# Performance work log

Measured on AMD Instinct MI355X. Metric: run time of the kernel, lower is better.

## Reference

```python
import jax, jax.numpy as jnp
import numpy as np

A, D, H, NACT = 8, 128, 64, 16  # n_agents, input_shape, rnn_hidden_dim, n_actions
B = 16384


def setup_inputs() -> dict:
    key = jax.random.key(0)
    ks = jax.random.split(key, 12)
    s = 1.0 / np.sqrt(H)
    si = 1.0 / np.sqrt(D)
    inp = {
        'inputs': jax.random.normal(ks[0], (B * A, D), dtype=jnp.float32),
        'hidden_state': jax.random.normal(ks[1], (B, A, H), dtype=jnp.float32),
        # stacked per-agent (non-shared) weights, PyTorch default-init scale
        'W1': jax.random.uniform(ks[2], (A, H, D), jnp.float32, -si, si),
        'b1': jax.random.uniform(ks[3], (A, H), jnp.float32, -si, si),
        'W_ih': jax.random.uniform(ks[4], (A, 3 * H, H), jnp.float32, -s, s),
        'b_ih': jax.random.uniform(ks[5], (A, 3 * H), jnp.float32, -s, s),
        'W_hh': jax.random.uniform(ks[6], (A, 3 * H, H), jnp.float32, -s, s),
        'b_hh': jax.random.uniform(ks[7], (A, 3 * H), jnp.float32, -s, s),
        'W2': jax.random.uniform(ks[8], (A, NACT, H), jnp.float32, -s, s),
        'b2': jax.random.uniform(ks[9], (A, NACT), jnp.float32, -s, s),
    }
    return inp


def reference(inputs, hidden_state, W1, b1, W_ih, b_ih, W_hh, b_hh, W2, b2):
    x = inputs.reshape(-1, A, D)                 # [B, A, D]
    h = hidden_state.reshape(-1, A, H)           # [B, A, H]
    # fc1 + ReLU, batched over agents
    z1 = jax.nn.relu(jnp.einsum('bad,ahd->bah', x, W1) + b1)
    # GRUCell (PyTorch convention: gates r, z, n)
    gi = jnp.einsum('bah,agh->bag', z1, W_ih) + b_ih   # [B, A, 3H]
    gh = jnp.einsum('bah,agh->bag', h, W_hh) + b_hh
    i_r, i_z, i_n = jnp.split(gi, 3, axis=-1)
    h_r, h_z, h_n = jnp.split(gh, 3, axis=-1)
    r = jax.nn.sigmoid(i_r + h_r)
    z = jax.nn.sigmoid(i_z + h_z)
    n = jnp.tanh(i_n + r * h_n)
    h_new = (1.0 - z) * n + z * h                # [B, A, H]
    # fc2
    q = jnp.einsum('bah,anh->ban', h_new, W2) + b2   # [B, A, NACT]
    # match torch: cat(qs, dim=-1).view(-1, n_actions) == reshape [B*A, NACT]
    return q.reshape(-1, NACT), h_new
```

## Files before the change

### kernel.cpp

```cpp
#include <hip/hip_runtime.h>
#include <hip/hip_bf16.h>
#include <cstddef>

#define NAGENT 8
#define DIN    128
#define HID    64
#define NACT   16

typedef __attribute__((ext_vector_type(8))) short bf16x8;
typedef __attribute__((ext_vector_type(4))) float f32x4;

__device__ __forceinline__ short f2bf(float f) {
    __hip_bfloat16 h = __float2bfloat16(f);
    union { __hip_bfloat16 h; short s; } u; u.h = h;
    return u.s;
}
__device__ __forceinline__ float sigmoid_f(float v) { return 1.0f / (1.0f + __expf(-v)); }
__device__ __forceinline__ float tanh_f(float v) {
    v = fminf(fmaxf(v, -15.0f), 15.0f);
    float e = __expf(2.0f * v);
    return (e - 1.0f) / (e + 1.0f);
}
__device__ __forceinline__ bf16x8 cvt8pair(float4 v0, float4 v1) {
    bf16x8 r;
    r[0] = f2bf(v0.x); r[1] = f2bf(v0.y); r[2] = f2bf(v0.z); r[3] = f2bf(v0.w);
    r[4] = f2bf(v1.x); r[5] = f2bf(v1.y); r[6] = f2bf(v1.z); r[7] = f2bf(v1.w);
    return r;
}

extern "C" __global__ void __launch_bounds__(256)
conv_weights_packed(const float* __restrict__ W1, const float* __restrict__ Wih,
                    const float* __restrict__ Whh, const float* __restrict__ W2,
                    short* __restrict__ ws)
{
    const int a = blockIdx.y;
    const int c = blockIdx.x * 256 + threadIdx.x;
    if (c >= 4224) return;
    const int lane = c & 63, lr = lane & 15, lk = lane >> 4;
    const float* src;
    if (c < 1024) {
        int n = c >> 8, k = (c >> 6) & 3;
        src = W1 + a * 8192 + (n * 16 + lr) * 128 + k * 32 + lk * 8;
    } else if (c < 2560) {
        int idx = (c - 1024) >> 6;
        int g = idx >> 3, n = (idx >> 1) & 3, kk = idx & 1;
        src = Wih + a * 12288 + (g * 64 + n * 16 + lr) * 64 + kk * 32 + lk * 8;
    } else if (c < 4096) {
        int idx = (c - 2560) >> 6;
        int g = idx >> 3, n = (idx >> 1) & 3, kk = idx & 1;
        src = Whh + a * 12288 + (g * 64 + n * 16 + lr) * 64 + kk * 32 + lk * 8;
    } else {
        int kk = (c - 4096) >> 6;
        src = W2 + a * 1024 + lr * 64 + kk * 32 + lk * 8;
    }
    float4 v0 = ((const float4*)src)[0];
    float4 v1 = ((const float4*)src)[1];
    bf16x8 o = cvt8pair(v0, v1);
    *(bf16x8*)(ws + (size_t)a * 33792 + (size_t)c * 8) = o;
}

extern "C" __global__ void __launch_bounds__(256, 4)
rnn_main(const float* __restrict__ x,
         const float* __restrict__ hin,
         const float* __restrict__ b1, const float* __restrict__ bih,
         const float* __restrict__ bhh, const float* __restrict__ b2,
         const short* __restrict__ wsp,
         float* __restrict__ qout,
         float* __restrict__ hout)
{
    const int bid  = blockIdx.x;
    const int a    = bid & 7;
    const int t    = threadIdx.x;
    const int wid  = t >> 6;
    const int lane = t & 63;
    const int lr   = lane & 15;
    const int lk   = lane >> 4;

    __shared__ short zs[4 * 1024];
    char* zb = (char*)(zs + wid * 1024);

    const short* wsA = wsp + (size_t)a * 33792;
    const int tile = (bid >> 3) * 4 + wid;
    const int arow = tile * 16 + lr;

    const float* xrow = x + ((size_t)arow * NAGENT + a) * DIN + lk * 8;
    const float* hrow = hin + ((size_t)arow * NAGENT + a) * HID + lk * 8;
    bf16x8 hf0 = cvt8pair(*(const float4*)(hrow),      *(const float4*)(hrow + 4));
    bf16x8 hf1 = cvt8pair(*(const float4*)(hrow + 32), *(const float4*)(hrow + 36));

    {
        f32x4 acc1[4];
        #pragma unroll
        for (int n = 0; n < 4; ++n) {
            float bv = b1[a * HID + n * 16 + lr];
            acc1[n] = (f32x4){bv, bv, bv, bv};
        }
        #pragma unroll
        for (int k = 0; k < 4; ++k) {
            bf16x8 xk = cvt8pair(*(const float4*)(xrow + k * 32),
                                 *(const float4*)(xrow + k * 32 + 4));
            #pragma unroll
            for (int n = 0; n < 4; ++n) {
                bf16x8 wb = *(const bf16x8*)(wsA + ((n * 4 + k) * 64 + lane) * 8);
                acc1[n] = __builtin_amdgcn_mfma_f32_16x16x32_bf16(xk, wb, acc1[n], 0, 0, 0);
            }
        }
        #pragma unroll
        for (int n = 0; n < 4; ++n)
            #pragma unroll
            for (int j = 0; j < 4; ++j) {
                int row = lk * 4 + j, col = n * 16 + lr;
                *(short*)(zb + row * 128 + ((col * 2) ^ ((row & 7) << 4))) =
                    f2bf(fmaxf(acc1[n][j], 0.0f));
            }
    }

    bf16x8 za0 = *(const bf16x8*)(zb + lr * 128 + ((0 * 64 + lk * 16) ^ ((lr & 7) << 4)));
    bf16x8 za1 = *(const bf16x8*)(zb + lr * 128 + ((1 * 64 + lk * 16) ^ ((lr & 7) << 4)));

    #pragma unroll 1
    for (int n = 0; n < 4; ++n) {
        float bhr = bhh[a * 192 +   0 + n * 16 + lr];
        float bhz = bhh[a * 192 +  64 + n * 16 + lr];
        float bhn = bhh[a * 192 + 128 + n * 16 + lr];
        f32x4 aHr = (f32x4){bhr, bhr, bhr, bhr};
        f32x4 aHz = (f32x4){bhz, bhz, bhz, bhz};
        f32x4 aHn = (f32x4){bhn, bhn, bhn, bhn};
        #pragma unroll
        for (int kk = 0; kk < 2; ++kk) {
            bf16x8 hfk = kk ? hf1 : hf0;
            bf16x8 whr = *(const bf16x8*)(wsA + 20480 + (((0 * 4 + n) * 2 + kk) * 64 + lane) * 8);
            bf16x8 whz = *(const bf16x8*)(wsA + 20480 + (((1 * 4 + n) * 2 + kk) * 64 + lane) * 8);
            bf16x8 whn = *(const bf16x8*)(wsA + 20480 + (((2 * 4 + n) * 2 + kk) * 64 + lane) * 8);
            aHr = __builtin_amdgcn_mfma_f32_16x16x32_bf16(hfk, whr, aHr, 0, 0, 0);
            aHz = __builtin_amdgcn_mfma_f32_16x16x32_bf16(hfk, whz, aHz, 0, 0, 0);
            aHn = __builtin_amdgcn_mfma_f32_16x16x32_bf16(hfk, whn, aHn, 0, 0, 0);
        }

        float bir = bih[a * 192 +   0 + n * 16 + lr];
        float biz = bih[a * 192 +  64 + n * 16 + lr];
        float bin_ = bih[a * 192 + 128 + n * 16 + lr];
        f32x4 aIr = (f32x4){bir, bir, bir, bir};
        f32x4 aIz = (f32x4){biz, biz, biz, biz};
        f32x4 aIn = (f32x4){bin_, bin_, bin_, bin_};
        #pragma unroll
        for (int kk = 0; kk < 2; ++kk) {
            bf16x8 zak = kk ? za1 : za0;
            bf16x8 wir = *(const bf16x8*)(wsA + 8192 + (((0 * 4 + n) * 2 + kk) * 64 + lane) * 8);
            bf16x8 wiz = *(const bf16x8*)(wsA + 8192 + (((1 * 4 + n) * 2 + kk) * 64 + lane) * 8);
            bf16x8 win = *(const bf16x8*)(wsA + 8192 + (((2 * 4 + n) * 2 + kk) * 64 + lane) * 8);
            aIr = __builtin_amdgcn_mfma_f32_16x16x32_bf16(zak, wir, aIr, 0, 0, 0);
            aIz = __builtin_amdgcn_mfma_f32_16x16x32_bf16(zak, wiz, aIz, 0, 0, 0);
            aIn = __builtin_amdgcn_mfma_f32_16x16x32_bf16(zak, win, aIn, 0, 0, 0);
        }

        #pragma unroll
        for (int j = 0; j < 4; ++j) {
            int row = lk * 4 + j, col = n * 16 + lr;
            float hp = hin[((size_t)(tile * 16 + row) * NAGENT + a) * HID + col];
            float r  = sigmoid_f(aIr[j] + aHr[j]);
            float zv = sigmoid_f(aIz[j] + aHz[j]);
            float nn = tanh_f(aIn[j] + r * aHn[j]);
            float hv = (1.0f - zv) * nn + zv * hp;
            hout[((size_t)(tile * 16 + row) * NAGENT + a) * HID + col] = hv;
            *(short*)(zb + row * 128 + ((col * 2) ^ ((row & 7) << 4))) = f2bf(hv);
        }
    }

    {
        float bq = b2[a * NACT + lr];
        f32x4 q = (f32x4){bq, bq, bq, bq};
        bf16x8 ha0 = *(const bf16x8*)(zb + lr * 128 + ((0 * 64 + lk * 16) ^ ((lr & 7) << 4)));
        bf16x8 ha1 = *(const bf16x8*)(zb + lr * 128 + ((1 * 64 + lk * 16) ^ ((lr & 7) << 4)));
        bf16x8 w2f0 = *(const bf16x8*)(wsA + 32768 + (0 * 64 + lane) * 8);
        bf16x8 w2f1 = *(const bf16x8*)(wsA + 32768 + (1 * 64 + lane) * 8);
        q = __builtin_amdgcn_mfma_f32_16x16x32_bf16(ha0, w2f0, q, 0, 0, 0);
        q = __builtin_amdgcn_mfma_f32_16x16x32_bf16(ha1, w2f1, q, 0, 0, 0);
        #pragma unroll
        for (int j = 0; j < 4; ++j)
            qout[((size_t)(tile * 16 + lk * 4 + j) * NAGENT + a) * NACT + lr] = q[j];
    }
}

extern "C" void kernel_launch(void* const* d_in, const int* in_sizes, int n_in,
                              void* d_out, int out_size, void* d_ws, size_t ws_size,
                              hipStream_t stream)
{
    const float* x   = (const float*)d_in[0];
    const float* hin = (const float*)d_in[1];
    const float* W1  = (const float*)d_in[2];
    const float* b1  = (const float*)d_in[3];
    const float* Wih = (const float*)d_in[4];
    const float* bih = (const float*)d_in[5];
    const float* Whh = (const float*)d_in[6];
    const float* bhh = (const float*)d_in[7];
    const float* W2  = (const float*)d_in[8];
    const float* b2  = (const float*)d_in[9];

    const int B = in_sizes[0] / (NAGENT * DIN);

    float* qout = (float*)d_out;
    float* hout = (float*)d_out + (size_t)B * NAGENT * NACT;

    short* wsp = (short*)d_ws;

    conv_weights_packed<<<dim3(17, NAGENT), 256, 0, stream>>>(W1, Wih, Whh, W2, wsp);

    dim3 grid((B / 64) * NAGENT);
    rnn_main<<<grid, 256, 0, stream>>>(x, hin, b1, bih, bhh, b2, wsp, qout, hout);
}
```

Before: 48.82 us.

## Switch GRU kernel to 32x32x16 MFMA with 32-row tiles per wave

```diff
diff --git a/kernel.cpp b/kernel.cpp
--- a/kernel.cpp
+++ b/kernel.cpp
@@ -7,8 +7,9 @@
 #define HID    64
 #define NACT   16
 
-typedef __attribute__((ext_vector_type(8))) short bf16x8;
-typedef __attribute__((ext_vector_type(4))) float f32x4;
+typedef __attribute__((ext_vector_type(8)))  short bf16x8;
+typedef __attribute__((ext_vector_type(4)))  float f32x4;
+typedef __attribute__((ext_vector_type(16))) float f32x16;
 
 __device__ __forceinline__ short f2bf(float f) {
     __hip_bfloat16 h = __float2bfloat16(f);
@@ -36,22 +37,24 @@
     const int a = blockIdx.y;
     const int c = blockIdx.x * 256 + threadIdx.x;
     if (c >= 4224) return;
-    const int lane = c & 63, lr = lane & 15, lk = lane >> 4;
+    const int lane  = c & 63;
+    const int chunk = c >> 6;
+    const int l31 = lane & 31, lkk = lane >> 5;
     const float* src;
-    if (c < 1024) {
-        int n = c >> 8, k = (c >> 6) & 3;
-        src = W1 + a * 8192 + (n * 16 + lr) * 128 + k * 32 + lk * 8;
-    } else if (c < 2560) {
-        int idx = (c - 1024) >> 6;
-        int g = idx >> 3, n = (idx >> 1) & 3, kk = idx & 1;
-        src = Wih + a * 12288 + (g * 64 + n * 16 + lr) * 64 + kk * 32 + lk * 8;
-    } else if (c < 4096) {
-        int idx = (c - 2560) >> 6;
-        int g = idx >> 3, n = (idx >> 1) & 3, kk = idx & 1;
-        src = Whh + a * 12288 + (g * 64 + n * 16 + lr) * 64 + kk * 32 + lk * 8;
+    if (chunk < 16) {
+        int n = chunk >> 3, i = chunk & 7;
+        src = W1 + a * 8192 + (n * 32 + l31) * 128 + i * 16 + lkk * 8;
+    } else if (chunk < 40) {
+        int idx = chunk - 16;
+        int g = idx >> 3, cb = (idx >> 2) & 1, ks = idx & 3;
+        src = Wih + a * 12288 + (g * 64 + cb * 32 + l31) * 64 + ks * 16 + lkk * 8;
+    } else if (chunk < 64) {
+        int idx = chunk - 40;
+        int g = idx >> 3, cb = (idx >> 2) & 1, ks = idx & 3;
+        src = Whh + a * 12288 + (g * 64 + cb * 32 + l31) * 64 + ks * 16 + lkk * 8;
     } else {
-        int kk = (c - 4096) >> 6;
-        src = W2 + a * 1024 + lr * 64 + kk * 32 + lk * 8;
+        int kk = chunk - 64;
+        src = W2 + a * 1024 + (lane & 15) * 64 + kk * 32 + (lane >> 4) * 8;
     }
     float4 v0 = ((const float4*)src)[0];
     float4 v1 = ((const float4*)src)[1];
@@ -59,7 +62,7 @@
     *(bf16x8*)(ws + (size_t)a * 33792 + (size_t)c * 8) = o;
 }
 
-extern "C" __global__ void __launch_bounds__(256, 4)
+extern "C" __global__ void __launch_bounds__(256, 2)
 rnn_main(const float* __restrict__ x,
          const float* __restrict__ hin,
          const float* __restrict__ b1, const float* __restrict__ bih,
@@ -73,112 +76,138 @@
     const int t    = threadIdx.x;
     const int wid  = t >> 6;
     const int lane = t & 63;
-    const int lr   = lane & 15;
-    const int lk   = lane >> 4;
-
-    __shared__ short zs[4 * 1024];
-    char* zb = (char*)(zs + wid * 1024);
+    const int l31  = lane & 31;
+    const int lkk  = lane >> 5;
+
+    __shared__ short zs[4 * 2048];
+    char* zb = (char*)(zs + wid * 2048);
 
     const short* wsA = wsp + (size_t)a * 33792;
-    const int tile = (bid >> 3) * 4 + wid;
-    const int arow = tile * 16 + lr;
-
-    const float* xrow = x + ((size_t)arow * NAGENT + a) * DIN + lk * 8;
-    const float* hrow = hin + ((size_t)arow * NAGENT + a) * HID + lk * 8;
-    bf16x8 hf0 = cvt8pair(*(const float4*)(hrow),      *(const float4*)(hrow + 4));
-    bf16x8 hf1 = cvt8pair(*(const float4*)(hrow + 32), *(const float4*)(hrow + 36));
+    const int rbase = ((bid >> 3) * 4 + wid) * 32;
+    const int arow  = rbase + l31;
+
+    const float* xrow = x + ((size_t)arow * NAGENT + a) * DIN + lkk * 8;
+    const float* hrow = hin + ((size_t)arow * NAGENT + a) * HID + lkk * 8;
+
+    bf16x8 hf[4];
+    #pragma unroll
+    for (int ks = 0; ks < 4; ++ks)
+        hf[ks] = cvt8pair(*(const float4*)(hrow + ks * 16),
+                          *(const float4*)(hrow + ks * 16 + 4));
 
     {
-        f32x4 acc1[4];
-        #pragma unroll
-        for (int n = 0; n < 4; ++n) {
-            float bv = b1[a * HID + n * 16 + lr];
-            acc1[n] = (f32x4){bv, bv, bv, bv};
-        }
-        #pragma unroll
-        for (int k = 0; k < 4; ++k) {
-            bf16x8 xk = cvt8pair(*(const float4*)(xrow + k * 32),
-                                 *(const float4*)(xrow + k * 32 + 4));
-            #pragma unroll
-            for (int n = 0; n < 4; ++n) {
-                bf16x8 wb = *(const bf16x8*)(wsA + ((n * 4 + k) * 64 + lane) * 8);
-                acc1[n] = __builtin_amdgcn_mfma_f32_16x16x32_bf16(xk, wb, acc1[n], 0, 0, 0);
-            }
-        }
-        #pragma unroll
-        for (int n = 0; n < 4; ++n)
-            #pragma unroll
-            for (int j = 0; j < 4; ++j) {
-                int row = lk * 4 + j, col = n * 16 + lr;
-                *(short*)(zb + row * 128 + ((col * 2) ^ ((row & 7) << 4))) =
-                    f2bf(fmaxf(acc1[n][j], 0.0f));
-            }
-    }
-
-    bf16x8 za0 = *(const bf16x8*)(zb + lr * 128 + ((0 * 64 + lk * 16) ^ ((lr & 7) << 4)));
-    bf16x8 za1 = *(const bf16x8*)(zb + lr * 128 + ((1 * 64 + lk * 16) ^ ((lr & 7) << 4)));
+        float bv0 = b1[a * HID + l31];
+        float bv1 = b1[a * HID + 32 + l31];
+        f32x16 acc0, acc1;
+        #pragma unroll
+        for (int r = 0; r < 16; ++r) { acc0[r] = bv0; acc1[r] = bv1; }
+        #pragma unroll
+        for (int i = 0; i < 8; ++i) {
+            bf16x8 xa = cvt8pair(*(const float4*)(xrow + i * 16),
+                                 *(const float4*)(xrow + i * 16 + 4));
+            bf16x8 w0 = *(const bf16x8*)(wsA + ((0 * 8 + i) * 64 + lane) * 8);
+            bf16x8 w1 = *(const bf16x8*)(wsA + ((1 * 8 + i) * 64 + lane) * 8);
+            acc0 = __builtin_amdgcn_mfma_f32_32x32x16_bf16(xa, w0, acc0, 0, 0, 0);
+            acc1 = __builtin_amdgcn_mfma_f32_32x32x16_bf16(xa, w1, acc1, 0, 0, 0);
+        }
+        #pragma unroll
+        for (int r = 0; r < 16; ++r) {
+            int row = (r & 3) + 8 * (r >> 2) + 4 * lkk;
+            int c0 = l31, c1 = 32 + l31;
+            *(short*)(zb + row * 128 + ((c0 * 2) ^ ((row & 7) << 4))) =
+                f2bf(fmaxf(acc0[r], 0.0f));
+            *(short*)(zb + row * 128 + ((c1 * 2) ^ ((row & 7) << 4))) =
+                f2bf(fmaxf(acc1[r], 0.0f));
+        }
+    }
+
+    bf16x8 za[4];
+    #pragma unroll
+    for (int ks = 0; ks < 4; ++ks)
+        za[ks] = *(const bf16x8*)(zb + l31 * 128 +
+                                  ((ks * 32 + lkk * 16) ^ ((l31 & 7) << 4)));
 
     #pragma unroll 1
-    for (int n = 0; n < 4; ++n) {
-        float bhr = bhh[a * 192 +   0 + n * 16 + lr];
-        float bhz = bhh[a * 192 +  64 + n * 16 + lr];
-        float bhn = bhh[a * 192 + 128 + n * 16 + lr];
-        f32x4 aHr = (f32x4){bhr, bhr, bhr, bhr};
-        f32x4 aHz = (f32x4){bhz, bhz, bhz, bhz};
-        f32x4 aHn = (f32x4){bhn, bhn, bhn, bhn};
-        #pragma unroll
-        for (int kk = 0; kk < 2; ++kk) {
-            bf16x8 hfk = kk ? hf1 : hf0;
-            bf16x8 whr = *(const bf16x8*)(wsA + 20480 + (((0 * 4 + n) * 2 + kk) * 64 + lane) * 8);
-            bf16x8 whz = *(const bf16x8*)(wsA + 20480 + (((1 * 4 + n) * 2 + kk) * 64 + lane) * 8);
-            bf16x8 whn = *(const bf16x8*)(wsA + 20480 + (((2 * 4 + n) * 2 + kk) * 64 + lane) * 8);
-            aHr = __builtin_amdgcn_mfma_f32_16x16x32_bf16(hfk, whr, aHr, 0, 0, 0);
-            aHz = __builtin_amdgcn_mfma_f32_16x16x32_bf16(hfk, whz, aHz, 0, 0, 0);
-            aHn = __builtin_amdgcn_mfma_f32_16x16x32_bf16(hfk, whn, aHn, 0, 0, 0);
-        }
-
-        float bir = bih[a * 192 +   0 + n * 16 + lr];
-        float biz = bih[a * 192 +  64 + n * 16 + lr];
-        float bin_ = bih[a * 192 + 128 + n * 16 + lr];
-        f32x4 aIr = (f32x4){bir, bir, bir, bir};
-        f32x4 aIz = (f32x4){biz, biz, biz, biz};
-        f32x4 aIn = (f32x4){bin_, bin_, bin_, bin_};
-        #pragma unroll
-        for (int kk = 0; kk < 2; ++kk) {
-            bf16x8 zak = kk ? za1 : za0;
-            bf16x8 wir = *(const bf16x8*)(wsA + 8192 + (((0 * 4 + n) * 2 + kk) * 64 + lane) * 8);
-            bf16x8 wiz = *(const bf16x8*)(wsA + 8192 + (((1 * 4 + n) * 2 + kk) * 64 + lane) * 8);
-            bf16x8 win = *(const bf16x8*)(wsA + 8192 + (((2 * 4 + n) * 2 + kk) * 64 + lane) * 8);
-            aIr = __builtin_amdgcn_mfma_f32_16x16x32_bf16(zak, wir, aIr, 0, 0, 0);
-            aIz = __builtin_amdgcn_mfma_f32_16x16x32_bf16(zak, wiz, aIz, 0, 0, 0);
-            aIn = __builtin_amdgcn_mfma_f32_16x16x32_bf16(zak, win, aIn, 0, 0, 0);
-        }
-
-        #pragma unroll
-        for (int j = 0; j < 4; ++j) {
-            int row = lk * 4 + j, col = n * 16 + lr;
-            float hp = hin[((size_t)(tile * 16 + row) * NAGENT + a) * HID + col];
-            float r  = sigmoid_f(aIr[j] + aHr[j]);
-            float zv = sigmoid_f(aIz[j] + aHz[j]);
-            float nn = tanh_f(aIn[j] + r * aHn[j]);
-            float hv = (1.0f - zv) * nn + zv * hp;
-            hout[((size_t)(tile * 16 + row) * NAGENT + a) * HID + col] = hv;
-            *(short*)(zb + row * 128 + ((col * 2) ^ ((row & 7) << 4))) = f2bf(hv);
+    for (int cb = 0; cb < 2; ++cb) {
+        const int col = cb * 32 + l31;
+        f32x16 rv, zv;
+
+        {
+            float bh = bhh[a * 192 + 0 * 64 + col];
+            float bi = bih[a * 192 + 0 * 64 + col];
+            f32x16 aH, aI;
+            #pragma unroll
+            for (int r = 0; r < 16; ++r) { aH[r] = bh; aI[r] = bi; }
+            #pragma unroll
+            for (int ks = 0; ks < 4; ++ks) {
+                bf16x8 wh = *(const bf16x8*)(wsA + ((40 + (0 * 2 + cb) * 4 + ks) * 64 + lane) * 8);
+                bf16x8 wi = *(const bf16x8*)(wsA + ((16 + (0 * 2 + cb) * 4 + ks) * 64 + lane) * 8);
+                aH = __builtin_amdgcn_mfma_f32_32x32x16_bf16(hf[ks], wh, aH, 0, 0, 0);
+                aI = __builtin_amdgcn_mfma_f32_32x32x16_bf16(za[ks], wi, aI, 0, 0, 0);
+            }
+            #pragma unroll
+            for (int r = 0; r < 16; ++r) rv[r] = sigmoid_f(aI[r] + aH[r]);
+        }
+        {
+            float bh = bhh[a * 192 + 1 * 64 + col];
+            float bi = bih[a * 192 + 1 * 64 + col];
+            f32x16 aH, aI;
+            #pragma unroll
+            for (int r = 0; r < 16; ++r) { aH[r] = bh; aI[r] = bi; }
+            #pragma unroll
+            for (int ks = 0; ks < 4; ++ks) {
+                bf16x8 wh = *(const bf16x8*)(wsA + ((40 + (1 * 2 + cb) * 4 + ks) * 64 + lane) * 8);
+                bf16x8 wi = *(const bf16x8*)(wsA + ((16 + (1 * 2 + cb) * 4 + ks) * 64 + lane) * 8);
+                aH = __builtin_amdgcn_mfma_f32_32x32x16_bf16(hf[ks], wh, aH, 0, 0, 0);
+                aI = __builtin_amdgcn_mfma_f32_32x32x16_bf16(za[ks], wi, aI, 0, 0, 0);
+            }
+            #pragma unroll
+            for (int r = 0; r < 16; ++r) zv[r] = sigmoid_f(aI[r] + aH[r]);
+        }
+        {
+            float bh = bhh[a * 192 + 2 * 64 + col];
+            float bi = bih[a * 192 + 2 * 64 + col];
+            f32x16 aH, aI;
+            #pragma unroll
+            for (int r = 0; r < 16; ++r) { aH[r] = bh; aI[r] = bi; }
+            #pragma unroll
+            for (int ks = 0; ks < 4; ++ks) {
+                bf16x8 wh = *(const bf16x8*)(wsA + ((40 + (2 * 2 + cb) * 4 + ks) * 64 + lane) * 8);
+                bf16x8 wi = *(const bf16x8*)(wsA + ((16 + (2 * 2 + cb) * 4 + ks) * 64 + lane) * 8);
+                aH = __builtin_amdgcn_mfma_f32_32x32x16_bf16(hf[ks], wh, aH, 0, 0, 0);
+                aI = __builtin_amdgcn_mfma_f32_32x32x16_bf16(za[ks], wi, aI, 0, 0, 0);
+            }
+            #pragma unroll
+            for (int r = 0; r < 16; ++r) {
+                int row = (r & 3) + 8 * (r >> 2) + 4 * lkk;
+                float hp = hin[((size_t)(rbase + row) * NAGENT + a) * HID + col];
+                float nn = tanh_f(aI[r] + rv[r] * aH[r]);
+                float hv = (1.0f - zv[r]) * nn + zv[r] * hp;
+                hout[((size_t)(rbase + row) * NAGENT + a) * HID + col] = hv;
+                *(short*)(zb + row * 128 + ((col * 2) ^ ((row & 7) << 4))) = f2bf(hv);
+            }
         }
     }
 
     {
+        const int lr = lane & 15, lk4 = lane >> 4;
         float bq = b2[a * NACT + lr];
-        f32x4 q = (f32x4){bq, bq, bq, bq};
-        bf16x8 ha0 = *(const bf16x8*)(zb + lr * 128 + ((0 * 64 + lk * 16) ^ ((lr & 7) << 4)));
-        bf16x8 ha1 = *(const bf16x8*)(zb + lr * 128 + ((1 * 64 + lk * 16) ^ ((lr & 7) << 4)));
-        bf16x8 w2f0 = *(const bf16x8*)(wsA + 32768 + (0 * 64 + lane) * 8);
-        bf16x8 w2f1 = *(const bf16x8*)(wsA + 32768 + (1 * 64 + lane) * 8);
-        q = __builtin_amdgcn_mfma_f32_16x16x32_bf16(ha0, w2f0, q, 0, 0, 0);
-        q = __builtin_amdgcn_mfma_f32_16x16x32_bf16(ha1, w2f1, q, 0, 0, 0);
-        #pragma unroll
-        for (int j = 0; j < 4; ++j)
-            qout[((size_t)(tile * 16 + lk * 4 + j) * NAGENT + a) * NACT + lr] = q[j];
+        bf16x8 w2f0 = *(const bf16x8*)(wsA + ((64 + 0) * 64 + lane) * 8);
+        bf16x8 w2f1 = *(const bf16x8*)(wsA + ((64 + 1) * 64 + lane) * 8);
+        #pragma unroll
+        for (int h = 0; h < 2; ++h) {
+            int zr = h * 16 + lr;
+            bf16x8 ha0 = *(const bf16x8*)(zb + zr * 128 +
+                          ((0 * 64 + lk4 * 16) ^ ((lr & 7) << 4)));
+            bf16x8 ha1 = *(const bf16x8*)(zb + zr * 128 +
+                          ((1 * 64 + lk4 * 16) ^ ((lr & 7) << 4)));
+            f32x4 q = (f32x4){bq, bq, bq, bq};
+            q = __builtin_amdgcn_mfma_f32_16x16x32_bf16(ha0, w2f0, q, 0, 0, 0);
+            q = __builtin_amdgcn_mfma_f32_16x16x32_bf16(ha1, w2f1, q, 0, 0, 0);
+            #pragma unroll
+            for (int j = 0; j < 4; ++j)
+                qout[((size_t)(rbase + h * 16 + lk4 * 4 + j) * NAGENT + a) * NACT + lr] = q[j];
+        }
     }
 }
 
@@ -206,6 +235,6 @@
 
     conv_weights_packed<<<dim3(17, NAGENT), 256, 0, stream>>>(W1, Wih, Whh, W2, wsp);
 
-    dim3 grid((B / 64) * NAGENT);
+    dim3 grid((B / 128) * NAGENT);
     rnn_main<<<grid, 256, 0, stream>>>(x, hin, b1, bih, bhh, b2, wsp, qout, hout);
 }
```

Measured after the change: 61.61 us. +26.2%, slower.

## Stage per-agent weights in LDS via async global-to-LDS loads shared across waves

Applied to the files above, without the earlier changes.

```diff
diff --git a/kernel.cpp b/kernel.cpp
--- a/kernel.cpp
+++ b/kernel.cpp
@@ -26,6 +26,11 @@
     r[0] = f2bf(v0.x); r[1] = f2bf(v0.y); r[2] = f2bf(v0.z); r[3] = f2bf(v0.w);
     r[4] = f2bf(v1.x); r[5] = f2bf(v1.y); r[6] = f2bf(v1.z); r[7] = f2bf(v1.w);
     return r;
+}
+__device__ __forceinline__ void gload_lds16(const void* g, void* l) {
+    __builtin_amdgcn_global_load_lds(
+        (const __attribute__((address_space(1))) unsigned int*)g,
+        (__attribute__((address_space(3))) unsigned int*)l, 16, 0, 0);
 }
 
 extern "C" __global__ void __launch_bounds__(256)
@@ -76,6 +81,7 @@
     const int lr   = lane & 15;
     const int lk   = lane >> 4;
 
+    __shared__ short wbuf[6144];
     __shared__ short zs[4 * 1024];
     char* zb = (char*)(zs + wid * 1024);
 
@@ -85,70 +91,100 @@
 
     const float* xrow = x + ((size_t)arow * NAGENT + a) * DIN + lk * 8;
     const float* hrow = hin + ((size_t)arow * NAGENT + a) * HID + lk * 8;
+
+    gload_lds16(wsA + (size_t)(wid * 2 + 0) * 512 + lane * 8, wbuf + (wid * 2 + 0) * 512);
+    gload_lds16(wsA + (size_t)(wid * 2 + 1) * 512 + lane * 8, wbuf + (wid * 2 + 1) * 512);
+
+    bf16x8 xf[4];
+    #pragma unroll
+    for (int k = 0; k < 4; ++k)
+        xf[k] = cvt8pair(*(const float4*)(xrow + k * 32),
+                         *(const float4*)(xrow + k * 32 + 4));
     bf16x8 hf0 = cvt8pair(*(const float4*)(hrow),      *(const float4*)(hrow + 4));
     bf16x8 hf1 = cvt8pair(*(const float4*)(hrow + 32), *(const float4*)(hrow + 36));
 
-    {
-        f32x4 acc1[4];
-        #pragma unroll
-        for (int n = 0; n < 4; ++n) {
-            float bv = b1[a * HID + n * 16 + lr];
-            acc1[n] = (f32x4){bv, bv, bv, bv};
-        }
-        #pragma unroll
-        for (int k = 0; k < 4; ++k) {
-            bf16x8 xk = cvt8pair(*(const float4*)(xrow + k * 32),
-                                 *(const float4*)(xrow + k * 32 + 4));
-            #pragma unroll
-            for (int n = 0; n < 4; ++n) {
-                bf16x8 wb = *(const bf16x8*)(wsA + ((n * 4 + k) * 64 + lane) * 8);
-                acc1[n] = __builtin_amdgcn_mfma_f32_16x16x32_bf16(xk, wb, acc1[n], 0, 0, 0);
-            }
-        }
-        #pragma unroll
-        for (int n = 0; n < 4; ++n)
-            #pragma unroll
-            for (int j = 0; j < 4; ++j) {
-                int row = lk * 4 + j, col = n * 16 + lr;
-                *(short*)(zb + row * 128 + ((col * 2) ^ ((row & 7) << 4))) =
-                    f2bf(fmaxf(acc1[n][j], 0.0f));
-            }
-    }
+    f32x4 acc1[4];
+    #pragma unroll
+    for (int n = 0; n < 4; ++n) {
+        float bv = b1[a * HID + n * 16 + lr];
+        acc1[n] = (f32x4){bv, bv, bv, bv};
+    }
+
+    __syncthreads();
+
+    #pragma unroll
+    for (int k = 0; k < 4; ++k)
+        #pragma unroll
+        for (int n = 0; n < 2; ++n) {
+            bf16x8 wb = *(const bf16x8*)(wbuf + ((n * 4 + k) * 64 + lane) * 8);
+            acc1[n] = __builtin_amdgcn_mfma_f32_16x16x32_bf16(xf[k], wb, acc1[n], 0, 0, 0);
+        }
+    __syncthreads();
+
+    gload_lds16(wsA + (size_t)(8 + wid * 2 + 0) * 512 + lane * 8, wbuf + (wid * 2 + 0) * 512);
+    gload_lds16(wsA + (size_t)(8 + wid * 2 + 1) * 512 + lane * 8, wbuf + (wid * 2 + 1) * 512);
+    __syncthreads();
+
+    #pragma unroll
+    for (int k = 0; k < 4; ++k)
+        #pragma unroll
+        for (int n = 2; n < 4; ++n) {
+            bf16x8 wb = *(const bf16x8*)(wbuf + (((n * 4 + k) - 8) * 64 + lane) * 8);
+            acc1[n] = __builtin_amdgcn_mfma_f32_16x16x32_bf16(xf[k], wb, acc1[n], 0, 0, 0);
+        }
+    #pragma unroll
+    for (int n = 0; n < 4; ++n)
+        #pragma unroll
+        for (int j = 0; j < 4; ++j) {
+            int row = lk * 4 + j, col = n * 16 + lr;
+            *(short*)(zb + row * 128 + ((col * 2) ^ ((row & 7) << 4))) =
+                f2bf(fmaxf(acc1[n][j], 0.0f));
+        }
 
     bf16x8 za0 = *(const bf16x8*)(zb + lr * 128 + ((0 * 64 + lk * 16) ^ ((lr & 7) << 4)));
     bf16x8 za1 = *(const bf16x8*)(zb + lr * 128 + ((1 * 64 + lk * 16) ^ ((lr & 7) << 4)));
 
     #pragma unroll 1
     for (int n = 0; n < 4; ++n) {
+        __syncthreads();
+        #pragma unroll
+        for (int si = 0; si < 3; ++si) {
+            int s = wid + si * 4;
+            int round = (s < 6) ? (16 + ((s >> 1) * 4 + n) * 2 + (s & 1))
+                                : (40 + (((s - 6) >> 1) * 4 + n) * 2 + ((s - 6) & 1));
+            gload_lds16(wsA + (size_t)round * 512 + lane * 8, wbuf + s * 512);
+        }
+        float hp[4];
+        #pragma unroll
+        for (int j = 0; j < 4; ++j)
+            hp[j] = hin[((size_t)(tile * 16 + lk * 4 + j) * NAGENT + a) * HID + n * 16 + lr];
         float bhr = bhh[a * 192 +   0 + n * 16 + lr];
         float bhz = bhh[a * 192 +  64 + n * 16 + lr];
         float bhn = bhh[a * 192 + 128 + n * 16 + lr];
+        float bir = bih[a * 192 +   0 + n * 16 + lr];
+        float biz = bih[a * 192 +  64 + n * 16 + lr];
+        float bin_ = bih[a * 192 + 128 + n * 16 + lr];
+        __syncthreads();
+
         f32x4 aHr = (f32x4){bhr, bhr, bhr, bhr};
         f32x4 aHz = (f32x4){bhz, bhz, bhz, bhz};
         f32x4 aHn = (f32x4){bhn, bhn, bhn, bhn};
+        f32x4 aIr = (f32x4){bir, bir, bir, bir};
+        f32x4 aIz = (f32x4){biz, biz, biz, biz};
+        f32x4 aIn = (f32x4){bin_, bin_, bin_, bin_};
         #pragma unroll
         for (int kk = 0; kk < 2; ++kk) {
             bf16x8 hfk = kk ? hf1 : hf0;
-            bf16x8 whr = *(const bf16x8*)(wsA + 20480 + (((0 * 4 + n) * 2 + kk) * 64 + lane) * 8);
-            bf16x8 whz = *(const bf16x8*)(wsA + 20480 + (((1 * 4 + n) * 2 + kk) * 64 + lane) * 8);
-            bf16x8 whn = *(const bf16x8*)(wsA + 20480 + (((2 * 4 + n) * 2 + kk) * 64 + lane) * 8);
+            bf16x8 zak = kk ? za1 : za0;
+            bf16x8 wir = *(const bf16x8*)(wbuf + ((0 * 2 + kk) * 64 + lane) * 8);
+            bf16x8 wiz = *(const bf16x8*)(wbuf + ((1 * 2 + kk) * 64 + lane) * 8);
+            bf16x8 win = *(const bf16x8*)(wbuf + ((2 * 2 + kk) * 64 + lane) * 8);
+            bf16x8 whr = *(const bf16x8*)(wbuf + ((6 + 0 * 2 + kk) * 64 + lane) * 8);
+            bf16x8 whz = *(const bf16x8*)(wbuf + ((6 + 1 * 2 + kk) * 64 + lane) * 8);
+            bf16x8 whn = *(const bf16x8*)(wbuf + ((6 + 2 * 2 + kk) * 64 + lane) * 8);
             aHr = __builtin_amdgcn_mfma_f32_16x16x32_bf16(hfk, whr, aHr, 0, 0, 0);
             aHz = __builtin_amdgcn_mfma_f32_16x16x32_bf16(hfk, whz, aHz, 0, 0, 0);
             aHn = __builtin_amdgcn_mfma_f32_16x16x32_bf16(hfk, whn, aHn, 0, 0, 0);
-        }
-
-        float bir = bih[a * 192 +   0 + n * 16 + lr];
-        float biz = bih[a * 192 +  64 + n * 16 + lr];
-        float bin_ = bih[a * 192 + 128 + n * 16 + lr];
-        f32x4 aIr = (f32x4){bir, bir, bir, bir};
-        f32x4 aIz = (f32x4){biz, biz, biz, biz};
-        f32x4 aIn = (f32x4){bin_, bin_, bin_, bin_};
-        #pragma unroll
-        for (int kk = 0; kk < 2; ++kk) {
-            bf16x8 zak = kk ? za1 : za0;
-            bf16x8 wir = *(const bf16x8*)(wsA + 8192 + (((0 * 4 + n) * 2 + kk) * 64 + lane) * 8);
-            bf16x8 wiz = *(const bf16x8*)(wsA + 8192 + (((1 * 4 + n) * 2 + kk) * 64 + lane) * 8);
-            bf16x8 win = *(const bf16x8*)(wsA + 8192 + (((2 * 4 + n) * 2 + kk) * 64 + lane) * 8);
             aIr = __builtin_amdgcn_mfma_f32_16x16x32_bf16(zak, wir, aIr, 0, 0, 0);
             aIz = __builtin_amdgcn_mfma_f32_16x16x32_bf16(zak, wiz, aIz, 0, 0, 0);
             aIn = __builtin_amdgcn_mfma_f32_16x16x32_bf16(zak, win, aIn, 0, 0, 0);
@@ -157,11 +193,10 @@
         #pragma unroll
         for (int j = 0; j < 4; ++j) {
             int row = lk * 4 + j, col = n * 16 + lr;
-            float hp = hin[((size_t)(tile * 16 + row) * NAGENT + a) * HID + col];
             float r  = sigmoid_f(aIr[j] + aHr[j]);
             float zv = sigmoid_f(aIz[j] + aHz[j]);
             float nn = tanh_f(aIn[j] + r * aHn[j]);
-            float hv = (1.0f - zv) * nn + zv * hp;
+            float hv = (1.0f - zv) * nn + zv * hp[j];
             hout[((size_t)(tile * 16 + row) * NAGENT + a) * HID + col] = hv;
             *(short*)(zb + row * 128 + ((col * 2) ^ ((row & 7) << 4))) = f2bf(hv);
         }
```

After: 48.71 us. Within noise of the previous version (-0.2%).

## Split fused RNN kernel into fc1 and GRU kernels staging z1 in output buffer

Applied to the files above, without the earlier changes.

```diff
diff --git a/kernel.cpp b/kernel.cpp
--- a/kernel.cpp
+++ b/kernel.cpp
@@ -15,11 +15,14 @@
     union { __hip_bfloat16 h; short s; } u; u.h = h;
     return u.s;
 }
+__device__ __forceinline__ float bf2f(unsigned short u) {
+    union { unsigned u; float f; } v; v.u = ((unsigned)u) << 16; return v.f;
+}
 __device__ __forceinline__ float sigmoid_f(float v) { return 1.0f / (1.0f + __expf(-v)); }
 __device__ __forceinline__ float tanh_f(float v) {
     v = fminf(fmaxf(v, -15.0f), 15.0f);
     float e = __expf(2.0f * v);
-    return (e - 1.0f) / (e + 1.0f);
+    return 1.0f - 2.0f / (e + 1.0f);
 }
 __device__ __forceinline__ bf16x8 cvt8pair(float4 v0, float4 v1) {
     bf16x8 r;
@@ -59,14 +62,10 @@
     *(bf16x8*)(ws + (size_t)a * 33792 + (size_t)c * 8) = o;
 }
 
+
 extern "C" __global__ void __launch_bounds__(256, 4)
-rnn_main(const float* __restrict__ x,
-         const float* __restrict__ hin,
-         const float* __restrict__ b1, const float* __restrict__ bih,
-         const float* __restrict__ bhh, const float* __restrict__ b2,
-         const short* __restrict__ wsp,
-         float* __restrict__ qout,
-         float* __restrict__ hout)
+fc1_kernel(const float* __restrict__ x, const float* __restrict__ b1,
+           const short* __restrict__ wsp, float* __restrict__ hout)
 {
     const int bid  = blockIdx.x;
     const int a    = bid & 7;
@@ -84,39 +83,69 @@
     const int arow = tile * 16 + lr;
 
     const float* xrow = x + ((size_t)arow * NAGENT + a) * DIN + lk * 8;
+
+    f32x4 acc1[4];
+    #pragma unroll
+    for (int n = 0; n < 4; ++n) {
+        float bv = b1[a * HID + n * 16 + lr];
+        acc1[n] = (f32x4){bv, bv, bv, bv};
+    }
+    #pragma unroll
+    for (int k = 0; k < 4; ++k) {
+        bf16x8 xk = cvt8pair(*(const float4*)(xrow + k * 32),
+                             *(const float4*)(xrow + k * 32 + 4));
+        #pragma unroll
+        for (int n = 0; n < 4; ++n) {
+            bf16x8 wb = *(const bf16x8*)(wsA + ((n * 4 + k) * 64 + lane) * 8);
+            acc1[n] = __builtin_amdgcn_mfma_f32_16x16x32_bf16(xk, wb, acc1[n], 0, 0, 0);
+        }
+    }
+    #pragma unroll
+    for (int n = 0; n < 4; ++n)
+        #pragma unroll
+        for (int j = 0; j < 4; ++j) {
+            int row = lk * 4 + j, col = n * 16 + lr;
+            *(short*)(zb + row * 128 + ((col * 2) ^ ((row & 7) << 4))) =
+                f2bf(fmaxf(acc1[n][j], 0.0f));
+        }
+    bf16x8 za0 = *(const bf16x8*)(zb + lr * 128 + ((0 * 64 + lk * 16) ^ ((lr & 7) << 4)));
+    bf16x8 za1 = *(const bf16x8*)(zb + lr * 128 + ((1 * 64 + lk * 16) ^ ((lr & 7) << 4)));
+
+    char* slot = (char*)hout +
+                 (((size_t)(tile * 16 + (lane >> 3)) * NAGENT + a) << 8) + (lane & 7) * 16;
+    *(bf16x8*)slot = za0;
+    *(bf16x8*)(slot + 128) = za1;
+}
+
+extern "C" __global__ void __launch_bounds__(256, 4)
+gru_kernel(const float* __restrict__ hin, const float* __restrict__ bih,
+           const float* __restrict__ bhh, const float* __restrict__ b2,
+           const short* __restrict__ wsp, float* __restrict__ qout,
+           float* __restrict__ hout)
+{
+    const int bid  = blockIdx.x;
+    const int a    = bid & 7;
+    const int t    = threadIdx.x;
+    const int wid  = t >> 6;
+    const int lane = t & 63;
+    const int lr   = lane & 15;
+    const int lk   = lane >> 4;
+
+    __shared__ short zs[4 * 1024];
+    char* zb = (char*)(zs + wid * 1024);
+
+    const short* wsA = wsp + (size_t)a * 33792;
+    const int tile = (bid >> 3) * 4 + wid;
+    const int arow = tile * 16 + lr;
+
+    const char* slot = (const char*)hout +
+                 (((size_t)(tile * 16 + (lane >> 3)) * NAGENT + a) << 8) + (lane & 7) * 16;
+    bf16x8 za0 = *(const bf16x8*)slot;
+    bf16x8 za1 = *(const bf16x8*)(slot + 128);
+
     const float* hrow = hin + ((size_t)arow * NAGENT + a) * HID + lk * 8;
     bf16x8 hf0 = cvt8pair(*(const float4*)(hrow),      *(const float4*)(hrow + 4));
     bf16x8 hf1 = cvt8pair(*(const float4*)(hrow + 32), *(const float4*)(hrow + 36));
-
-    {
-        f32x4 acc1[4];
-        #pragma unroll
-        for (int n = 0; n < 4; ++n) {
-            float bv = b1[a * HID + n * 16 + lr];
-            acc1[n] = (f32x4){bv, bv, bv, bv};
-        }
-        #pragma unroll
-        for (int k = 0; k < 4; ++k) {
-            bf16x8 xk = cvt8pair(*(const float4*)(xrow + k * 32),
-                                 *(const float4*)(xrow + k * 32 + 4));
-            #pragma unroll
-            for (int n = 0; n < 4; ++n) {
-                bf16x8 wb = *(const bf16x8*)(wsA + ((n * 4 + k) * 64 + lane) * 8);
-                acc1[n] = __builtin_amdgcn_mfma_f32_16x16x32_bf16(xk, wb, acc1[n], 0, 0, 0);
-            }
-        }
-        #pragma unroll
-        for (int n = 0; n < 4; ++n)
-            #pragma unroll
-            for (int j = 0; j < 4; ++j) {
-                int row = lk * 4 + j, col = n * 16 + lr;
-                *(short*)(zb + row * 128 + ((col * 2) ^ ((row & 7) << 4))) =
-                    f2bf(fmaxf(acc1[n][j], 0.0f));
-            }
-    }
-
-    bf16x8 za0 = *(const bf16x8*)(zb + lr * 128 + ((0 * 64 + lk * 16) ^ ((lr & 7) << 4)));
-    bf16x8 za1 = *(const bf16x8*)(zb + lr * 128 + ((1 * 64 + lk * 16) ^ ((lr & 7) << 4)));
 
     #pragma unroll 1
     for (int n = 0; n < 4; ++n) {
@@ -162,7 +191,6 @@
             float zv = sigmoid_f(aIz[j] + aHz[j]);
             float nn = tanh_f(aIn[j] + r * aHn[j]);
             float hv = (1.0f - zv) * nn + zv * hp;
-            hout[((size_t)(tile * 16 + row) * NAGENT + a) * HID + col] = hv;
             *(short*)(zb + row * 128 + ((col * 2) ^ ((row & 7) << 4))) = f2bf(hv);
         }
     }
@@ -179,6 +207,24 @@
         #pragma unroll
         for (int j = 0; j < 4; ++j)
             qout[((size_t)(tile * 16 + lk * 4 + j) * NAGENT + a) * NACT + lr] = q[j];
+    }
+
+    {
+        int row = lane >> 2;
+        int c0  = (lane & 3) * 4;
+        float* hb = hout + ((size_t)(tile * 16 + row) * NAGENT + a) * HID + c0;
+        #pragma unroll
+        for (int i = 0; i < 4; ++i) {
+            int cb = (c0 + i * 16) * 2;
+            unsigned long long v =
+                *(const unsigned long long*)(zb + row * 128 + (cb ^ ((row & 7) << 4)));
+            float4 o;
+            o.x = bf2f((unsigned short)(v));
+            o.y = bf2f((unsigned short)(v >> 16));
+            o.z = bf2f((unsigned short)(v >> 32));
+            o.w = bf2f((unsigned short)(v >> 48));
+            *(float4*)(hb + i * 16) = o;
+        }
     }
 }
 
@@ -207,5 +253,6 @@
     conv_weights_packed<<<dim3(17, NAGENT), 256, 0, stream>>>(W1, Wih, Whh, W2, wsp);
 
     dim3 grid((B / 64) * NAGENT);
-    rnn_main<<<grid, 256, 0, stream>>>(x, hin, b1, bih, bhh, b2, wsp, qout, hout);
-}
+    fc1_kernel<<<grid, 256, 0, stream>>>(x, b1, wsp, hout);
+    gru_kernel<<<grid, 256, 0, stream>>>(hin, bih, bhh, b2, wsp, qout, hout);
+}
```

Result: slower. 55.51 us (+13.7%).
